# Kernel tuning notes

Measured on AMD Instinct MI355X. Metric: run time of the kernel, lower is better.

## Reference

```python
import jax, jax.numpy as jnp
import numpy as np

N_NODES = 50000
N_EDGES = 800000
NODE_DIM = 64
EDGE_DIM = 32


def _glorot(key, shape):
    fan_in, fan_out = shape
    lim = (6.0 / (fan_in + fan_out)) ** 0.5
    return jax.random.uniform(key, shape, jnp.float32, -lim, lim)


def setup_inputs() -> dict:
    key = jax.random.key(0)
    ks = jax.random.split(key, 12)
    x = jax.random.normal(ks[0], (N_NODES, NODE_DIM), jnp.float32)
    edge_index = jax.random.randint(ks[1], (2, N_EDGES), 0, N_NODES, jnp.int64)
    edge_attr = jax.random.normal(ks[2], (N_EDGES, EDGE_DIM), jnp.float32)
    # edge_mlp: Linear(edge_dim + 2*node_dim -> node_dim), ReLU, Linear(node_dim -> node_dim)
    W1e = _glorot(ks[3], (EDGE_DIM + 2 * NODE_DIM, NODE_DIM))
    b1e = jnp.zeros((NODE_DIM,), jnp.float32)
    W2e = _glorot(ks[4], (NODE_DIM, NODE_DIM))
    b2e = jnp.zeros((NODE_DIM,), jnp.float32)
    # node_mlp: Linear(2*node_dim -> node_dim), ReLU, Linear(node_dim -> node_dim)
    W1n = _glorot(ks[5], (2 * NODE_DIM, NODE_DIM))
    b1n = jnp.zeros((NODE_DIM,), jnp.float32)
    W2n = _glorot(ks[6], (NODE_DIM, NODE_DIM))
    b2n = jnp.zeros((NODE_DIM,), jnp.float32)
    return {"x": x, "edge_index": edge_index, "edge_attr": edge_attr,
            "W1e": W1e, "b1e": b1e, "W2e": W2e, "b2e": b2e,
            "W1n": W1n, "b1n": b1n, "W2n": W2n, "b2n": b2n}


def reference(x, edge_index, edge_attr, W1e, b1e, W2e, b2e, W1n, b1n, W2n, b2n):
    row, col = edge_index[0], edge_index[1]
    # gather endpoint features: [E, node_dim] each
    edge_input = jnp.concatenate([x[row], x[col], edge_attr], axis=-1)  # [E, 2D+De]
    h = jax.nn.relu(edge_input @ W1e + b1e)
    edge_output = h @ W2e + b2e  # [E, D]
    # scatter-add into target nodes
    aggregated = jnp.zeros_like(x).at[col].add(edge_output)  # [N, D]
    node_input = jnp.concatenate([x, aggregated], axis=-1)  # [N, 2D]
    g = jax.nn.relu(node_input @ W1n + b1n)
    node_output = g @ W2n + b2n
    return jax.nn.relu(node_output + x)
```

## Files before the change

### kernel.cpp

```cpp
#include <hip/hip_runtime.h>

typedef float    f32x4 __attribute__((ext_vector_type(4)));
typedef short    s16x8 __attribute__((ext_vector_type(8)));
typedef unsigned u32x2 __attribute__((ext_vector_type(2)));
typedef unsigned u32x4 __attribute__((ext_vector_type(4)));

#define ND   64
#define DE   32
#define KN   128
#define KNP  136
#define K2P  72
#define WBP  40

__device__ __forceinline__ ushort f2bf(float f) {
  unsigned u = __float_as_uint(f);
  return (ushort)((u + 0x7fffu + ((u >> 16) & 1u)) >> 16);
}
__device__ __forceinline__ float relu_f(float v) { return v > 0.f ? v : 0.f; }
__device__ __forceinline__ unsigned cvtpk(float lo, float hi) {
  unsigned r;
  asm("v_cvt_pk_bf16_f32 %0, %1, %2" : "=v"(r) : "v"(lo), "v"(hi));
  return r;
}
__device__ __forceinline__ float bflo(unsigned u) { return __uint_as_float(u << 16); }
__device__ __forceinline__ float bfhi(unsigned u) { return __uint_as_float(u & 0xffff0000u); }

__launch_bounds__(256, 2)
__global__ void gc_pq(const float* __restrict__ x,
                      const float* __restrict__ W1e,
                      unsigned* __restrict__ PQ,
                      int N) {
  __shared__ ushort xl[64][K2P];
  __shared__ ushort wtA[ND][K2P];
  __shared__ ushort wtB[ND][K2P];

  const int t = threadIdx.x, lane = t & 63, w = t >> 6;
  const int l15 = lane & 15, lhi = lane >> 4, k8 = lhi * 8;

  for (int i = t; i < ND * ND; i += 256) {
    wtA[i & 63][i >> 6] = f2bf(W1e[i]);
    wtB[i & 63][i >> 6] = f2bf(W1e[(size_t)ND * ND + i]);
  }
  const int n0 = blockIdx.x * 64;
  #pragma unroll
  for (int i = 0; i < 4; ++i) {
    int chunk = t + i * 256;
    int r = chunk >> 4, p = chunk & 15;
    int node = n0 + r; if (node >= N) node = N - 1;
    f32x4 v = *(const f32x4*)(x + (size_t)node * ND + p * 4);
    unsigned* dst = (unsigned*)&xl[r][p * 4];
    dst[0] = cvtpk(v.x, v.y); dst[1] = cvtpk(v.z, v.w);
  }
  __syncthreads();

  const int strip = w * 16;
  const int ar = strip + l15;
  s16x8 a0 = *(const s16x8*)&xl[ar][k8];
  s16x8 a1 = *(const s16x8*)&xl[ar][32 + k8];

  f32x4 accP[4] = {}, accQ[4] = {};
  #pragma unroll
  for (int n = 0; n < 4; ++n) {
    s16x8 bA0 = *(const s16x8*)&wtA[n * 16 + l15][k8];
    s16x8 bA1 = *(const s16x8*)&wtA[n * 16 + l15][32 + k8];
    s16x8 bB0 = *(const s16x8*)&wtB[n * 16 + l15][k8];
    s16x8 bB1 = *(const s16x8*)&wtB[n * 16 + l15][32 + k8];
    accP[n] = __builtin_amdgcn_mfma_f32_16x16x32_bf16(a0, bA0, accP[n], 0, 0, 0);
    accP[n] = __builtin_amdgcn_mfma_f32_16x16x32_bf16(a1, bA1, accP[n], 0, 0, 0);
    accQ[n] = __builtin_amdgcn_mfma_f32_16x16x32_bf16(a0, bB0, accQ[n], 0, 0, 0);
    accQ[n] = __builtin_amdgcn_mfma_f32_16x16x32_bf16(a1, bB1, accQ[n], 0, 0, 0);
  }
  #pragma unroll
  for (int n = 0; n < 4; ++n) {
    #pragma unroll
    for (int j = 0; j < 4; ++j) {
      int node = n0 + strip + lhi * 4 + j;
      float rP = accP[n][j];  float pP = __shfl_xor(rP, 1);
      float rQ = accQ[n][j];  float pQ = __shfl_xor(rQ, 1);
      if (!(l15 & 1) && node < N) {
        unsigned dw = (unsigned)(n * 16 + l15) >> 1;
        PQ[(size_t)node * 64 + dw]      = cvtpk(rP, pP);
        PQ[(size_t)node * 64 + 32 + dw] = cvtpk(rQ, pQ);
      }
    }
  }
}

__launch_bounds__(256, 4)
__global__ void gc_edge_pq(const int* __restrict__ eidx,
                           const float* __restrict__ eattr,
                           const float* __restrict__ W1e, const float* __restrict__ b1e,
                           const unsigned* __restrict__ PQ,
                           unsigned* __restrict__ hsum,
                           float* __restrict__ deg,
                           int E, int ngroups) {
  __shared__ ushort   w1bt[ND][WBP];
  __shared__ unsigned hb[4][16][33];

  const int t = threadIdx.x, lane = t & 63, w = t >> 6;
  const int l15 = lane & 15, lhi = lane >> 4, k8 = lhi * 8;

  for (int i = t; i < DE * ND; i += 256)
    w1bt[i & 63][i >> 6] = f2bf(W1e[(size_t)KN * ND + i]);
  __syncthreads();

  s16x8 bfr[4];
  #pragma unroll
  for (int n = 0; n < 4; ++n) bfr[n] = *(const s16x8*)&w1bt[n * 16 + l15][k8];

  float bias[4];
  #pragma unroll
  for (int n = 0; n < 4; ++n) bias[n] = b1e[n * 16 + l15];

  const int ee4 = lhi;
  const int q16 = l15;

  const int wid = blockIdx.x * 4 + w;
  const int nw  = gridDim.x * 4;

  for (int g = wid; g < ngroups; g += nw) {
    const int e0 = g * 16;
    int myidx = 0;
    if (lane < 32)
      myidx = (lane < 16) ? eidx[e0 + lane] : eidx[E + e0 + (lane - 16)];

    int prow[4], pcol[4];
    #pragma unroll
    for (int m = 0; m < 4; ++m) {
      prow[m] = __shfl(myidx, m * 4 + ee4);
      pcol[m] = __shfl(myidx, 16 + m * 4 + ee4);
    }

    unsigned Pv[4][2], Qv[4][2];
    #pragma unroll
    for (int m = 0; m < 4; ++m) {
      const unsigned* pb = PQ + (size_t)prow[m] * 64;
      const unsigned* qb = PQ + (size_t)pcol[m] * 64 + 32;
      Pv[m][0] = pb[q16];      Pv[m][1] = pb[16 + q16];
      Qv[m][0] = qb[q16];      Qv[m][1] = qb[16 + q16];
    }

    const float* ap = eattr + ((size_t)e0 + l15) * DE + k8;
    f32x4 alo = __builtin_nontemporal_load((const f32x4*)ap);
    f32x4 ahi = __builtin_nontemporal_load((const f32x4*)(ap + 4));
    union { unsigned u[4]; s16x8 v; } af;
    af.u[0] = cvtpk(alo.x, alo.y); af.u[1] = cvtpk(alo.z, alo.w);
    af.u[2] = cvtpk(ahi.x, ahi.y); af.u[3] = cvtpk(ahi.z, ahi.w);

    f32x4 acc[4] = {};
    #pragma unroll
    for (int n = 0; n < 4; ++n)
      acc[n] = __builtin_amdgcn_mfma_f32_16x16x32_bf16(af.v, bfr[n], acc[n], 0, 0, 0);

    if (lane >= 16 && lane < 32) atomicAdd(&deg[myidx], 1.0f);

    #pragma unroll
    for (int n = 0; n < 4; ++n) {
      #pragma unroll
      for (int j = 0; j < 4; ++j) {
        float r = acc[n][j] + bias[n];
        float p = __shfl_xor(r, 1);
        if (!(l15 & 1)) hb[w][lhi * 4 + j][(n * 16 + l15) >> 1] = cvtpk(r, p);
      }
    }
    asm volatile("s_waitcnt lgkmcnt(0)" ::: "memory");

    #pragma unroll
    for (int m = 0; m < 4; ++m) {
      unsigned* hd = hsum + (size_t)pcol[m] * 32 + q16;
      #pragma unroll
      for (int h = 0; h < 2; ++h) {
        unsigned R  = hb[w][m * 4 + ee4][h * 16 + q16];
        unsigned Pu = Pv[m][h], Qu = Qv[m][h];
        float slo = relu_f(bflo(Pu) + bflo(Qu) + bflo(R));
        float shi = relu_f(bfhi(Pu) + bfhi(Qu) + bfhi(R));
        unsigned dw = cvtpk(slo, shi);
        asm volatile("global_atomic_pk_add_bf16 %0, %1, off"
                     :: "v"((uint64_t)(hd + h * 16)), "v"(dw) : "memory");
      }
    }
  }
}

__launch_bounds__(256, 2)
__global__ void gc_node(const float* __restrict__ x,
                        const ushort* __restrict__ hsum,
                        const float* __restrict__ deg,
                        const float* __restrict__ W2e, const float* __restrict__ b2e,
                        const float* __restrict__ W1n, const float* __restrict__ b1n,
                        const float* __restrict__ W2n, const float* __restrict__ b2n,
                        float* __restrict__ out, int N) {
  __shared__ ushort w2et[ND][K2P];
  __shared__ ushort w1nt[ND][KNP];
  __shared__ ushort w2nt[ND][K2P];
  __shared__ ushort in_lds[64][KNP];
  __shared__ ushort h_lds[64][K2P];

  const int t    = threadIdx.x;
  const int lane = t & 63;
  const int w    = t >> 6;
  const int l15  = lane & 15;
  const int lhi  = lane >> 4;
  const int k8   = lhi * 8;

  for (int i = t; i < 64 * ND; i += 256) w2et[i & 63][i >> 6] = f2bf(W2e[i]);
  for (int i = t; i < KN * ND; i += 256) w1nt[i & 63][i >> 6] = f2bf(W1n[i]);
  for (int i = t; i < 64 * ND; i += 256) w2nt[i & 63][i >> 6] = f2bf(W2n[i]);

  const int n0 = blockIdx.x * 64;
  #pragma unroll
  for (int i = 0; i < 4; ++i) {
    int chunk = t + i * 256;
    int r = chunk >> 4, p = chunk & 15;
    int node = n0 + r; if (node >= N) node = N - 1;
    f32x4 v = *(const f32x4*)(x + (size_t)node * ND + p * 4);
    unsigned* dst = (unsigned*)&in_lds[r][p * 4];
    dst[0] = cvtpk(v.x, v.y); dst[1] = cvtpk(v.z, v.w);
  }

  const int strip = w * 16;
  {
    int arow = strip + l15;
    int node = n0 + arow; if (node >= N) node = N - 1;
    const s16x8* ph = (const s16x8*)(hsum + (size_t)node * ND);
    s16x8 a0 = ph[lhi];
    s16x8 a1 = ph[4 + lhi];
    __syncthreads();
    f32x4 accg[4] = {};
    #pragma unroll
    for (int n = 0; n < 4; ++n) {
      s16x8 b0 = *(const s16x8*)&w2et[n * 16 + l15][k8];
      s16x8 b1 = *(const s16x8*)&w2et[n * 16 + l15][32 + k8];
      accg[n] = __builtin_amdgcn_mfma_f32_16x16x32_bf16(a0, b0, accg[n], 0, 0, 0);
      accg[n] = __builtin_amdgcn_mfma_f32_16x16x32_bf16(a1, b1, accg[n], 0, 0, 0);
    }
    #pragma unroll
    for (int n = 0; n < 4; ++n) {
      int d = n * 16 + l15;
      float b2 = b2e[d];
      #pragma unroll
      for (int j = 0; j < 4; ++j) {
        int r = strip + lhi * 4 + j;
        int node2 = n0 + r; if (node2 >= N) node2 = N - 1;
        float ag = accg[n][j] + deg[node2] * b2;
        in_lds[r][64 + d] = f2bf(ag);
      }
    }
  }
  __syncthreads();

  const int ar = strip + l15;
  f32x4 acc1[4] = {};
  #pragma unroll
  for (int ks = 0; ks < 4; ++ks) {
    s16x8 a = *(const s16x8*)&in_lds[ar][ks * 32 + k8];
    #pragma unroll
    for (int n = 0; n < 4; ++n) {
      s16x8 b = *(const s16x8*)&w1nt[n * 16 + l15][ks * 32 + k8];
      acc1[n] = __builtin_amdgcn_mfma_f32_16x16x32_bf16(a, b, acc1[n], 0, 0, 0);
    }
  }
  #pragma unroll
  for (int n = 0; n < 4; ++n) {
    int d = n * 16 + l15;
    float bias = b1n[d];
    #pragma unroll
    for (int j = 0; j < 4; ++j)
      h_lds[strip + lhi * 4 + j][d] = f2bf(relu_f(acc1[n][j] + bias));
  }
  __syncthreads();

  f32x4 acc2[4] = {};
  #pragma unroll
  for (int ks = 0; ks < 2; ++ks) {
    s16x8 a = *(const s16x8*)&h_lds[ar][ks * 32 + k8];
    #pragma unroll
    for (int n = 0; n < 4; ++n) {
      s16x8 b = *(const s16x8*)&w2nt[n * 16 + l15][ks * 32 + k8];
      acc2[n] = __builtin_amdgcn_mfma_f32_16x16x32_bf16(a, b, acc2[n], 0, 0, 0);
    }
  }
  #pragma unroll
  for (int n = 0; n < 4; ++n) {
    int d = n * 16 + l15;
    float bias = b2n[d];
    #pragma unroll
    for (int j = 0; j < 4; ++j) {
      int node = n0 + strip + lhi * 4 + j;
      if (node < N) {
        float xv = x[(size_t)node * ND + d];
        out[(size_t)node * ND + d] = relu_f(acc2[n][j] + bias + xv);
      }
    }
  }
}

extern "C" void kernel_launch(void* const* d_in, const int* in_sizes, int n_in,
                              void* d_out, int out_size, void* d_ws, size_t ws_size,
                              hipStream_t stream) {
  const float* x     = (const float*)d_in[0];
  const int*   eidx  = (const int*)d_in[1];
  const float* eattr = (const float*)d_in[2];
  const float* W1e   = (const float*)d_in[3];
  const float* b1e   = (const float*)d_in[4];
  const float* W2e   = (const float*)d_in[5];
  const float* b2e   = (const float*)d_in[6];
  const float* W1n   = (const float*)d_in[7];
  const float* b1n   = (const float*)d_in[8];
  const float* W2n   = (const float*)d_in[9];
  const float* b2n   = (const float*)d_in[10];
  float* out = (float*)d_out;

  const int N = in_sizes[0] / ND;
  const int E = in_sizes[1] / 2;

  char* ws = (char*)d_ws;
  unsigned* hsum = (unsigned*)ws;
  float*    deg  = (float*)(ws + (size_t)N * ND * 2);
  unsigned* PQ   = (unsigned*)(ws + (size_t)N * ND * 2 + (size_t)N * 4);

  hipMemsetAsync(ws, 0, (size_t)N * ND * 2 + (size_t)N * 4, stream);

  gc_pq<<<(N + 63) / 64, 256, 0, stream>>>(x, W1e, PQ, N);
  gc_edge_pq<<<2048, 256, 0, stream>>>(eidx, eattr, W1e, b1e, PQ,
                                       hsum, deg, E, E / 16);
  gc_node<<<(N + 63) / 64, 256, 0, stream>>>(x, (const ushort*)hsum, deg,
                                             W2e, b2e, W1n, b1n, W2n, b2n, out, N);
}
```

Before: 173.9 us.

## Bucket edges by destination window and accumulate in LDS instead of global atomics

Replaces the global bf16 packed-atomic scatter with a counting-sort pipeline: a degree histogram, a single-block prefix scan over 32-node windows, and a placement pass that writes (row, local col, edge id) records. The edge kernel then processes one destination window per block, caching Q rows in LDS, accumulating in fp32 LDS atomics, and writing hsum once per node. This removes contended global atomics and the hsum memset, and accumulates in fp32 rather than bf16. In exchange it adds three extra launches, a serial single-block scan, a record array round-trip and random eattr gathers.

Result: slower. 536.4 us (+208.4%).

```diff
diff --git a/kernel.cpp b/kernel.cpp
--- a/kernel.cpp
+++ b/kernel.cpp
@@ -11,6 +11,8 @@
 #define KNP  136
 #define K2P  72
 #define WBP  40
+#define WIN  32
+#define QS   68
 
 __device__ __forceinline__ ushort f2bf(float f) {
   unsigned u = __float_as_uint(f);
@@ -86,99 +88,153 @@
   }
 }
 
+__global__ void gc_hist(const int* __restrict__ eidx, float* __restrict__ deg, int E) {
+  int i = blockIdx.x * blockDim.x + threadIdx.x;
+  for (; i < E; i += gridDim.x * blockDim.x)
+    atomicAdd(&deg[eidx[E + i]], 1.0f);
+}
+
+__global__ void gc_prefix_w(const float* __restrict__ deg, int N, int NW,
+                            int* __restrict__ offset, int* __restrict__ cursor) {
+  __shared__ int wt[16], we[16];
+  __shared__ int srun, ctot;
+  const int t = threadIdx.x, lane = t & 63, w = t >> 6;
+  if (t == 0) srun = 0;
+  __syncthreads();
+  for (int base = 0; base < NW; base += 1024) {
+    int b = base + t;
+    int v = 0;
+    if (b < NW) {
+      int n0 = b * WIN, n1 = n0 + WIN; if (n1 > N) n1 = N;
+      for (int k = n0; k < n1; ++k) v += (int)deg[k];
+    }
+    int incl = v;
+    #pragma unroll
+    for (int d = 1; d < 64; d <<= 1) {
+      int u = __shfl_up(incl, d);
+      if (lane >= d) incl += u;
+    }
+    if (lane == 63) wt[w] = incl;
+    __syncthreads();
+    if (t == 0) {
+      int run = 0;
+      #pragma unroll
+      for (int k = 0; k < 16; ++k) { we[k] = run; run += wt[k]; }
+      ctot = run;
+    }
+    __syncthreads();
+    if (b < NW) { int ex = srun + we[w] + incl - v; offset[b] = ex; cursor[b] = ex; }
+    __syncthreads();
+    if (t == 0) srun += ctot;
+    __syncthreads();
+  }
+  if (t == 0) offset[NW] = srun;
+}
+
+__global__ void gc_place(const int* __restrict__ eidx, int* __restrict__ cursor,
+                         int2* __restrict__ recs, int E) {
+  int i = blockIdx.x * blockDim.x + threadIdx.x;
+  for (; i < E; i += gridDim.x * blockDim.x) {
+    int col = eidx[E + i];
+    int row = eidx[i];
+    int win = col >> 5;
+    int pos = atomicAdd(&cursor[win], 1);
+    recs[pos] = make_int2(row, ((col & (WIN - 1)) << 26) | i);
+  }
+}
+
 __launch_bounds__(256, 4)
-__global__ void gc_edge_pq(const int* __restrict__ eidx,
-                           const float* __restrict__ eattr,
-                           const float* __restrict__ W1e, const float* __restrict__ b1e,
-                           const unsigned* __restrict__ PQ,
-                           unsigned* __restrict__ hsum,
-                           float* __restrict__ deg,
-                           int E, int ngroups) {
-  __shared__ ushort   w1bt[ND][WBP];
-  __shared__ unsigned hb[4][16][33];
+__global__ void gc_edge_w(const float* __restrict__ eattr,
+                          const float* __restrict__ W1e, const float* __restrict__ b1e,
+                          const unsigned* __restrict__ PQ,
+                          const int2* __restrict__ recs,
+                          const int* __restrict__ offset,
+                          unsigned* __restrict__ hsum,
+                          int N) {
+  __shared__ ushort w1bt[ND][WBP];
+  __shared__ float  qwin[WIN][QS];
+  __shared__ float  accw[WIN][QS];
 
   const int t = threadIdx.x, lane = t & 63, w = t >> 6;
   const int l15 = lane & 15, lhi = lane >> 4, k8 = lhi * 8;
+  const int bkt = blockIdx.x, c0 = bkt * WIN;
 
   for (int i = t; i < DE * ND; i += 256)
     w1bt[i & 63][i >> 6] = f2bf(W1e[(size_t)KN * ND + i]);
+  for (int i = t; i < WIN * 32; i += 256) {
+    int r = i >> 5, dw = i & 31;
+    int node = c0 + r;
+    unsigned q = (node < N) ? PQ[(size_t)node * 64 + 32 + dw] : 0u;
+    qwin[r][2 * dw] = bflo(q); qwin[r][2 * dw + 1] = bfhi(q);
+  }
+  for (int i = t; i < WIN * 64; i += 256) accw[i >> 6][i & 63] = 0.f;
   __syncthreads();
 
   s16x8 bfr[4];
   #pragma unroll
   for (int n = 0; n < 4; ++n) bfr[n] = *(const s16x8*)&w1bt[n * 16 + l15][k8];
-
   float bias[4];
   #pragma unroll
   for (int n = 0; n < 4; ++n) bias[n] = b1e[n * 16 + l15];
 
-  const int ee4 = lhi;
-  const int q16 = l15;
-
-  const int wid = blockIdx.x * 4 + w;
-  const int nw  = gridDim.x * 4;
-
-  for (int g = wid; g < ngroups; g += nw) {
-    const int e0 = g * 16;
-    int myidx = 0;
-    if (lane < 32)
-      myidx = (lane < 16) ? eidx[e0 + lane] : eidx[E + e0 + (lane - 16)];
-
-    int prow[4], pcol[4];
-    #pragma unroll
-    for (int m = 0; m < 4; ++m) {
-      prow[m] = __shfl(myidx, m * 4 + ee4);
-      pcol[m] = __shfl(myidx, 16 + m * 4 + ee4);
-    }
-
-    unsigned Pv[4][2], Qv[4][2];
-    #pragma unroll
-    for (int m = 0; m < 4; ++m) {
-      const unsigned* pb = PQ + (size_t)prow[m] * 64;
-      const unsigned* qb = PQ + (size_t)pcol[m] * 64 + 32;
-      Pv[m][0] = pb[q16];      Pv[m][1] = pb[16 + q16];
-      Qv[m][0] = qb[q16];      Qv[m][1] = qb[16 + q16];
-    }
-
-    const float* ap = eattr + ((size_t)e0 + l15) * DE + k8;
+  const int start = offset[bkt], end = offset[bkt + 1];
+  const int nIter = (end - start + 63) >> 6;
+
+  for (int it = 0; it < nIter; ++it) {
+    const int eBase = start + it * 64 + w * 16;
+    int rx = 0, ry = 0;
+    if (lane < 16) {
+      int idx = eBase + lane;
+      if (idx >= end) idx = end - 1;
+      int2 rr = recs[idx];
+      rx = rr.x; ry = rr.y;
+    }
+    int erow[4], eloc[4];
+    #pragma unroll
+    for (int j = 0; j < 4; ++j) {
+      erow[j] = __shfl(rx, lhi * 4 + j);
+      eloc[j] = (int)((unsigned)__shfl(ry, lhi * 4 + j) >> 26);
+    }
+
+    unsigned pdw[4][4];
+    #pragma unroll
+    for (int j = 0; j < 4; ++j)
+      #pragma unroll
+      for (int n = 0; n < 4; ++n)
+        pdw[n][j] = PQ[(size_t)erow[j] * 64 + n * 8 + (l15 >> 1)];
+
+    int eid = __shfl(ry, l15) & 0x3FFFFFF;
+    const float* ap = eattr + (size_t)eid * DE + k8;
     f32x4 alo = __builtin_nontemporal_load((const f32x4*)ap);
     f32x4 ahi = __builtin_nontemporal_load((const f32x4*)(ap + 4));
     union { unsigned u[4]; s16x8 v; } af;
     af.u[0] = cvtpk(alo.x, alo.y); af.u[1] = cvtpk(alo.z, alo.w);
     af.u[2] = cvtpk(ahi.x, ahi.y); af.u[3] = cvtpk(ahi.z, ahi.w);
 
-    f32x4 acc[4] = {};
+    f32x4 rv[4] = {};
     #pragma unroll
     for (int n = 0; n < 4; ++n)
-      acc[n] = __builtin_amdgcn_mfma_f32_16x16x32_bf16(af.v, bfr[n], acc[n], 0, 0, 0);
-
-    if (lane >= 16 && lane < 32) atomicAdd(&deg[myidx], 1.0f);
-
-    #pragma unroll
-    for (int n = 0; n < 4; ++n) {
+      rv[n] = __builtin_amdgcn_mfma_f32_16x16x32_bf16(af.v, bfr[n], rv[n], 0, 0, 0);
+
+    #pragma unroll
+    for (int n = 0; n < 4; ++n) {
+      int d = n * 16 + l15;
       #pragma unroll
       for (int j = 0; j < 4; ++j) {
-        float r = acc[n][j] + bias[n];
-        float p = __shfl_xor(r, 1);
-        if (!(l15 & 1)) hb[w][lhi * 4 + j][(n * 16 + l15) >> 1] = cvtpk(r, p);
+        float pv = (l15 & 1) ? bfhi(pdw[n][j]) : bflo(pdw[n][j]);
+        float s = relu_f(rv[n][j] + bias[n] + pv + qwin[eloc[j]][d]);
+        if (eBase + lhi * 4 + j < end)
+          atomicAdd(&accw[eloc[j]][d], s);
       }
     }
-    asm volatile("s_waitcnt lgkmcnt(0)" ::: "memory");
-
-    #pragma unroll
-    for (int m = 0; m < 4; ++m) {
-      unsigned* hd = hsum + (size_t)pcol[m] * 32 + q16;
-      #pragma unroll
-      for (int h = 0; h < 2; ++h) {
-        unsigned R  = hb[w][m * 4 + ee4][h * 16 + q16];
-        unsigned Pu = Pv[m][h], Qu = Qv[m][h];
-        float slo = relu_f(bflo(Pu) + bflo(Qu) + bflo(R));
-        float shi = relu_f(bfhi(Pu) + bfhi(Qu) + bfhi(R));
-        unsigned dw = cvtpk(slo, shi);
-        asm volatile("global_atomic_pk_add_bf16 %0, %1, off"
-                     :: "v"((uint64_t)(hd + h * 16)), "v"(dw) : "memory");
-      }
-    }
+  }
+  __syncthreads();
+
+  for (int i = t; i < WIN * 32; i += 256) {
+    int r = i >> 5, dw = i & 31;
+    int node = c0 + r;
+    if (node < N)
+      hsum[(size_t)node * 32 + dw] = cvtpk(accw[r][2 * dw], accw[r][2 * dw + 1]);
   }
 }
 
@@ -311,19 +367,25 @@
   const float* b2n   = (const float*)d_in[10];
   float* out = (float*)d_out;
 
-  const int N = in_sizes[0] / ND;
-  const int E = in_sizes[1] / 2;
+  const int N  = in_sizes[0] / ND;
+  const int E  = in_sizes[1] / 2;
+  const int NW = (N + WIN - 1) / WIN;
 
   char* ws = (char*)d_ws;
-  unsigned* hsum = (unsigned*)ws;
-  float*    deg  = (float*)(ws + (size_t)N * ND * 2);
-  unsigned* PQ   = (unsigned*)(ws + (size_t)N * ND * 2 + (size_t)N * 4);
-
-  hipMemsetAsync(ws, 0, (size_t)N * ND * 2 + (size_t)N * 4, stream);
-
+  unsigned* hsum   = (unsigned*)ws;
+  float*    deg    = (float*)(ws + (size_t)N * ND * 2);
+  unsigned* PQ     = (unsigned*)(ws + (size_t)N * ND * 2 + (size_t)N * 4);
+  int*      offset = (int*)((char*)PQ + (size_t)N * 64 * 4);
+  int*      cursor = offset + (NW + 1);
+  int2*     recs   = (int2*)(cursor + NW);
+
+  hipMemsetAsync(deg, 0, (size_t)N * 4, stream);
+
+  gc_hist<<<1024, 256, 0, stream>>>(eidx, deg, E);
   gc_pq<<<(N + 63) / 64, 256, 0, stream>>>(x, W1e, PQ, N);
-  gc_edge_pq<<<2048, 256, 0, stream>>>(eidx, eattr, W1e, b1e, PQ,
-                                       hsum, deg, E, E / 16);
+  gc_prefix_w<<<1, 1024, 0, stream>>>(deg, N, NW, offset, cursor);
+  gc_place<<<1024, 256, 0, stream>>>(eidx, cursor, recs, E);
+  gc_edge_w<<<NW, 256, 0, stream>>>(eattr, W1e, b1e, PQ, recs, offset, hsum, N);
   gc_node<<<(N + 63) / 64, 256, 0, stream>>>(x, (const ushort*)hsum, deg,
                                              W2e, b2e, W1n, b1n, W2n, b2n, out, N);
 }
```

## Replace scatter-add atomics with per-node CSR gather via counting sort

Applied to the files above, without the earlier changes.

Builds a CSR index of edges grouped by destination node on every call, using a histogram, a three-stage scan and an atomic placement pass. The edge kernel then walks each destination node's edge list per wavefront and sums relu outputs in registers, writing hsum once per node instead of issuing bf16 atomic adds per edge. Degree now comes from offset differences rather than a float atomic counter. This removes the atomic contention and the hsum memset, but adds five extra launches and random gathers of eattr through recs, and it leaves wavefronts idle or imbalanced when node degrees vary.

Result: slower. 199.5 us (+14.7%).

```diff
diff --git a/kernel.cpp b/kernel.cpp
--- a/kernel.cpp
+++ b/kernel.cpp
@@ -2,8 +2,6 @@
 
 typedef float    f32x4 __attribute__((ext_vector_type(4)));
 typedef short    s16x8 __attribute__((ext_vector_type(8)));
-typedef unsigned u32x2 __attribute__((ext_vector_type(2)));
-typedef unsigned u32x4 __attribute__((ext_vector_type(4)));
 
 #define ND   64
 #define DE   32
@@ -86,19 +84,90 @@
   }
 }
 
+__global__ void gc_hist(const int* __restrict__ eidx, int* __restrict__ deg, int E) {
+  int i = blockIdx.x * blockDim.x + threadIdx.x;
+  for (; i < E; i += gridDim.x * blockDim.x)
+    atomicAdd(&deg[eidx[E + i]], 1);
+}
+
+__global__ void gc_scan1(const int* __restrict__ deg, int N,
+                         int* __restrict__ offset, int* __restrict__ bsum) {
+  __shared__ int wt[4], we[4];
+  const int t = threadIdx.x, lane = t & 63, w = t >> 6;
+  const int base = blockIdx.x * 1024 + t * 4;
+  int v0 = (base     < N) ? deg[base]     : 0;
+  int v1 = (base + 1 < N) ? deg[base + 1] : 0;
+  int v2 = (base + 2 < N) ? deg[base + 2] : 0;
+  int v3 = (base + 3 < N) ? deg[base + 3] : 0;
+  int s = v0 + v1 + v2 + v3;
+  int incl = s;
+  #pragma unroll
+  for (int d = 1; d < 64; d <<= 1) {
+    int u = __shfl_up(incl, d);
+    if (lane >= d) incl += u;
+  }
+  if (lane == 63) wt[w] = incl;
+  __syncthreads();
+  if (t == 0) {
+    int run = 0;
+    #pragma unroll
+    for (int k = 0; k < 4; ++k) { we[k] = run; run += wt[k]; }
+    bsum[blockIdx.x] = run;
+  }
+  __syncthreads();
+  int ex = we[w] + incl - s;
+  if (base     < N) offset[base]     = ex; ex += v0;
+  if (base + 1 < N) offset[base + 1] = ex; ex += v1;
+  if (base + 2 < N) offset[base + 2] = ex; ex += v2;
+  if (base + 3 < N) offset[base + 3] = ex;
+}
+
+__global__ void gc_scan2(int* __restrict__ bsum, int nb) {
+  int lane = threadIdx.x;
+  int v = (lane < nb) ? bsum[lane] : 0;
+  int incl = v;
+  #pragma unroll
+  for (int d = 1; d < 64; d <<= 1) {
+    int u = __shfl_up(incl, d);
+    if (lane >= d) incl += u;
+  }
+  if (lane < nb) bsum[lane] = incl - v;
+}
+
+__global__ void gc_scan3(int* __restrict__ offset, int* __restrict__ cursor,
+                         const int* __restrict__ bsum, int N, int E) {
+  int i = blockIdx.x * blockDim.x + threadIdx.x;
+  if (i < N) {
+    int o = offset[i] + bsum[i >> 10];
+    offset[i] = o; cursor[i] = o;
+  }
+  if (i == 0) offset[N] = E;
+}
+
+__global__ void gc_place(const int* __restrict__ eidx, int* __restrict__ cursor,
+                         int* __restrict__ recs, int E) {
+  int i = blockIdx.x * blockDim.x + threadIdx.x;
+  for (; i < E; i += gridDim.x * blockDim.x) {
+    int col = eidx[E + i];
+    int pos = atomicAdd(&cursor[col], 1);
+    recs[pos] = i;
+  }
+}
+
 __launch_bounds__(256, 4)
-__global__ void gc_edge_pq(const int* __restrict__ eidx,
-                           const float* __restrict__ eattr,
-                           const float* __restrict__ W1e, const float* __restrict__ b1e,
-                           const unsigned* __restrict__ PQ,
-                           unsigned* __restrict__ hsum,
-                           float* __restrict__ deg,
-                           int E, int ngroups) {
-  __shared__ ushort   w1bt[ND][WBP];
-  __shared__ unsigned hb[4][16][33];
+__global__ void gc_edge_n(const int* __restrict__ eidx,
+                          const float* __restrict__ eattr,
+                          const float* __restrict__ W1e, const float* __restrict__ b1e,
+                          const unsigned* __restrict__ PQ,
+                          const int* __restrict__ recs,
+                          const int* __restrict__ offset,
+                          unsigned* __restrict__ hsum,
+                          int N, int E) {
+  __shared__ ushort w1bt[ND][WBP];
 
   const int t = threadIdx.x, lane = t & 63, w = t >> 6;
   const int l15 = lane & 15, lhi = lane >> 4, k8 = lhi * 8;
+  const int sel = l15 & 1;
 
   for (int i = t; i < DE * ND; i += 256)
     w1bt[i & 63][i >> 6] = f2bf(W1e[(size_t)KN * ND + i]);
@@ -107,85 +176,89 @@
   s16x8 bfr[4];
   #pragma unroll
   for (int n = 0; n < 4; ++n) bfr[n] = *(const s16x8*)&w1bt[n * 16 + l15][k8];
-
   float bias[4];
   #pragma unroll
   for (int n = 0; n < 4; ++n) bias[n] = b1e[n * 16 + l15];
-
-  const int ee4 = lhi;
-  const int q16 = l15;
 
   const int wid = blockIdx.x * 4 + w;
   const int nw  = gridDim.x * 4;
 
-  for (int g = wid; g < ngroups; g += nw) {
-    const int e0 = g * 16;
-    int myidx = 0;
-    if (lane < 32)
-      myidx = (lane < 16) ? eidx[e0 + lane] : eidx[E + e0 + (lane - 16)];
-
-    int prow[4], pcol[4];
-    #pragma unroll
-    for (int m = 0; m < 4; ++m) {
-      prow[m] = __shfl(myidx, m * 4 + ee4);
-      pcol[m] = __shfl(myidx, 16 + m * 4 + ee4);
-    }
-
-    unsigned Pv[4][2], Qv[4][2];
-    #pragma unroll
-    for (int m = 0; m < 4; ++m) {
-      const unsigned* pb = PQ + (size_t)prow[m] * 64;
-      const unsigned* qb = PQ + (size_t)pcol[m] * 64 + 32;
-      Pv[m][0] = pb[q16];      Pv[m][1] = pb[16 + q16];
-      Qv[m][0] = qb[q16];      Qv[m][1] = qb[16 + q16];
-    }
-
-    const float* ap = eattr + ((size_t)e0 + l15) * DE + k8;
-    f32x4 alo = __builtin_nontemporal_load((const f32x4*)ap);
-    f32x4 ahi = __builtin_nontemporal_load((const f32x4*)(ap + 4));
-    union { unsigned u[4]; s16x8 v; } af;
-    af.u[0] = cvtpk(alo.x, alo.y); af.u[1] = cvtpk(alo.z, alo.w);
-    af.u[2] = cvtpk(ahi.x, ahi.y); af.u[3] = cvtpk(ahi.z, ahi.w);
-
-    f32x4 acc[4] = {};
-    #pragma unroll
-    for (int n = 0; n < 4; ++n)
-      acc[n] = __builtin_amdgcn_mfma_f32_16x16x32_bf16(af.v, bfr[n], acc[n], 0, 0, 0);
-
-    if (lane >= 16 && lane < 32) atomicAdd(&deg[myidx], 1.0f);
-
-    #pragma unroll
-    for (int n = 0; n < 4; ++n) {
+  for (int v = wid; v < N; v += nw) {
+    const int start = offset[v], end = offset[v + 1];
+
+    float bq0, bq1, bq2, bq3;
+    {
+      const unsigned* qb = PQ + (size_t)v * 64 + 32 + (l15 >> 1);
+      unsigned q0 = qb[0], q1 = qb[8], q2 = qb[16], q3 = qb[24];
+      bq0 = bias[0] + (sel ? bfhi(q0) : bflo(q0));
+      bq1 = bias[1] + (sel ? bfhi(q1) : bflo(q1));
+      bq2 = bias[2] + (sel ? bfhi(q2) : bflo(q2));
+      bq3 = bias[3] + (sel ? bfhi(q3) : bflo(q3));
+    }
+
+    float acc0 = 0.f, acc1 = 0.f, acc2 = 0.f, acc3 = 0.f;
+    for (int tb = start; tb < end; tb += 16) {
+      int eidL = 0, erowL = 0;
+      if (lane < 16) {
+        int ii = tb + lane; if (ii >= end) ii = end - 1;
+        eidL  = recs[ii];
+        erowL = eidx[eidL];
+      }
+      int erow[4];
+      #pragma unroll
+      for (int j = 0; j < 4; ++j) erow[j] = __shfl(erowL, lhi * 4 + j);
+
+      unsigned pdw[4][4];
       #pragma unroll
       for (int j = 0; j < 4; ++j) {
-        float r = acc[n][j] + bias[n];
-        float p = __shfl_xor(r, 1);
-        if (!(l15 & 1)) hb[w][lhi * 4 + j][(n * 16 + l15) >> 1] = cvtpk(r, p);
-      }
-    }
-    asm volatile("s_waitcnt lgkmcnt(0)" ::: "memory");
-
-    #pragma unroll
-    for (int m = 0; m < 4; ++m) {
-      unsigned* hd = hsum + (size_t)pcol[m] * 32 + q16;
+        const unsigned* pb = PQ + (size_t)erow[j] * 64 + (l15 >> 1);
+        pdw[0][j] = pb[0]; pdw[1][j] = pb[8]; pdw[2][j] = pb[16]; pdw[3][j] = pb[24];
+      }
+
+      int eidA = __shfl(eidL, l15);
+      const float* ap = eattr + (size_t)eidA * DE + k8;
+      f32x4 alo = __builtin_nontemporal_load((const f32x4*)ap);
+      f32x4 ahi = __builtin_nontemporal_load((const f32x4*)(ap + 4));
+      union { unsigned u[4]; s16x8 v; } af;
+      af.u[0] = cvtpk(alo.x, alo.y); af.u[1] = cvtpk(alo.z, alo.w);
+      af.u[2] = cvtpk(ahi.x, ahi.y); af.u[3] = cvtpk(ahi.z, ahi.w);
+
+      f32x4 rv[4] = {};
       #pragma unroll
-      for (int h = 0; h < 2; ++h) {
-        unsigned R  = hb[w][m * 4 + ee4][h * 16 + q16];
-        unsigned Pu = Pv[m][h], Qu = Qv[m][h];
-        float slo = relu_f(bflo(Pu) + bflo(Qu) + bflo(R));
-        float shi = relu_f(bfhi(Pu) + bfhi(Qu) + bfhi(R));
-        unsigned dw = cvtpk(slo, shi);
-        asm volatile("global_atomic_pk_add_bf16 %0, %1, off"
-                     :: "v"((uint64_t)(hd + h * 16)), "v"(dw) : "memory");
-      }
-    }
+      for (int n = 0; n < 4; ++n)
+        rv[n] = __builtin_amdgcn_mfma_f32_16x16x32_bf16(af.v, bfr[n], rv[n], 0, 0, 0);
+
+      const int rem = end - tb;
+      #pragma unroll
+      for (int n = 0; n < 4; ++n) {
+        float bqn = (n == 0) ? bq0 : (n == 1) ? bq1 : (n == 2) ? bq2 : bq3;
+        float sum = 0.f;
+        #pragma unroll
+        for (int j = 0; j < 4; ++j) {
+          float pv = sel ? bfhi(pdw[n][j]) : bflo(pdw[n][j]);
+          float s  = relu_f(rv[n][j] + bqn + pv);
+          if (lhi * 4 + j < rem) sum += s;
+        }
+        sum += __shfl_xor(sum, 16);
+        sum += __shfl_xor(sum, 32);
+        if (n == 0) acc0 += sum; else if (n == 1) acc1 += sum;
+        else if (n == 2) acc2 += sum; else acc3 += sum;
+      }
+    }
+
+    unsigned dw0 = cvtpk(acc0, __shfl_xor(acc0, 1));
+    unsigned dw1 = cvtpk(acc1, __shfl_xor(acc1, 1));
+    unsigned dw2 = cvtpk(acc2, __shfl_xor(acc2, 1));
+    unsigned dw3 = cvtpk(acc3, __shfl_xor(acc3, 1));
+    unsigned dwv = (lhi == 0) ? dw0 : (lhi == 1) ? dw1 : (lhi == 2) ? dw2 : dw3;
+    if (!sel) hsum[(size_t)v * 32 + lhi * 8 + (l15 >> 1)] = dwv;
   }
 }
 
 __launch_bounds__(256, 2)
 __global__ void gc_node(const float* __restrict__ x,
                         const ushort* __restrict__ hsum,
-                        const float* __restrict__ deg,
+                        const int* __restrict__ offset,
                         const float* __restrict__ W2e, const float* __restrict__ b2e,
                         const float* __restrict__ W1n, const float* __restrict__ b1n,
                         const float* __restrict__ W2n, const float* __restrict__ b2n,
@@ -242,7 +315,8 @@
       for (int j = 0; j < 4; ++j) {
         int r = strip + lhi * 4 + j;
         int node2 = n0 + r; if (node2 >= N) node2 = N - 1;
-        float ag = accg[n][j] + deg[node2] * b2;
+        float degf = (float)(offset[node2 + 1] - offset[node2]);
+        float ag = accg[n][j] + degf * b2;
         in_lds[r][64 + d] = f2bf(ag);
       }
     }
@@ -313,17 +387,26 @@
 
   const int N = in_sizes[0] / ND;
   const int E = in_sizes[1] / 2;
+  const int NB = (N + 1023) / 1024;
 
   char* ws = (char*)d_ws;
-  unsigned* hsum = (unsigned*)ws;
-  float*    deg  = (float*)(ws + (size_t)N * ND * 2);
-  unsigned* PQ   = (unsigned*)(ws + (size_t)N * ND * 2 + (size_t)N * 4);
-
-  hipMemsetAsync(ws, 0, (size_t)N * ND * 2 + (size_t)N * 4, stream);
-
+  unsigned* hsum   = (unsigned*)ws;
+  int*      deg    = (int*)(ws + (size_t)N * 128);
+  int*      offset = deg + N;
+  int*      cursor = offset + (N + 1);
+  int*      bsum   = cursor + N;
+  unsigned* PQ     = (unsigned*)(bsum + 64);
+  int*      recs   = (int*)(PQ + (size_t)N * 64);
+
+  hipMemsetAsync(deg, 0, (size_t)N * 4, stream);
+
+  gc_hist<<<1024, 256, 0, stream>>>(eidx, deg, E);
   gc_pq<<<(N + 63) / 64, 256, 0, stream>>>(x, W1e, PQ, N);
-  gc_edge_pq<<<2048, 256, 0, stream>>>(eidx, eattr, W1e, b1e, PQ,
-                                       hsum, deg, E, E / 16);
-  gc_node<<<(N + 63) / 64, 256, 0, stream>>>(x, (const ushort*)hsum, deg,
+  gc_scan1<<<NB, 256, 0, stream>>>(deg, N, offset, bsum);
+  gc_scan2<<<1, 64, 0, stream>>>(bsum, NB);
+  gc_scan3<<<(N + 255) / 256, 256, 0, stream>>>(offset, cursor, bsum, N, E);
+  gc_place<<<1024, 256, 0, stream>>>(eidx, cursor, recs, E);
+  gc_edge_n<<<2048, 256, 0, stream>>>(eidx, eattr, W1e, b1e, PQ, recs, offset, hsum, N, E);
+  gc_node<<<(N + 63) / 64, 256, 0, stream>>>(x, (const ushort*)hsum, offset,
                                              W2e, b2e, W1n, b1n, W2n, b2n, out, N);
 }
```
